# Performance work log

Measured on AMD Instinct MI355X. Metric: run time of the kernel, lower is better.

## Reference

```python
import jax, jax.numpy as jnp
import numpy as np

H = 512      # hidden_size (encoder_embed_dim)
K = 2        # kernel_size (neighbor window)
EPS = 1e-5   # LayerNorm eps

def _ln(x, g, b):
    m = jnp.mean(x, axis=-1, keepdims=True)
    v = jnp.mean(jnp.square(x - m), axis=-1, keepdims=True)
    return (x - m) * jax.lax.rsqrt(v + EPS) * g + b

def _shift_before(h, step):
    # pad `step` zero frames at the front of the seq dim (torch get_hidden_states_before)
    return jnp.pad(h, ((0, 0), (step, 0), (0, 0)))[:, :h.shape[1], :]

def _shift_after(h, step):
    # pad `step` zero frames at the end (torch get_hidden_states_after)
    return jnp.pad(h, ((0, 0), (0, step), (0, 0)))[:, step:, :]

def setup_inputs() -> dict:
    key = jax.random.key(0)
    ks = jax.random.split(key, 12)
    B, S = 32, 256
    s = 0.1  # module init: normal(mean=0, std=0.1)
    return {
        "word_inputs": jax.random.normal(ks[0], (B, S, H), jnp.float32),
        "mask": jnp.zeros((B, S), jnp.int32),  # 1 = padding
        "Wg": jax.random.normal(ks[1], (3 * H, 7 * H), jnp.float32) * s,   # norm_gate.weight.T
        "bg": jax.random.normal(ks[2], (7 * H,), jnp.float32) * s,         # norm_gate.bias
        "We_gate": jax.random.normal(ks[3], (H, 7 * H), jnp.float32) * s,  # emb_gate_linear.weight.T
        "We_trans": jax.random.normal(ks[4], (H, H), jnp.float32) * s,     # emb_trans.weight.T
        "be_trans": jax.random.normal(ks[5], (H,), jnp.float32) * s,
        "W1": jax.random.normal(ks[6], (H, 2 * H), jnp.float32) * (1.0 / np.sqrt(H)),
        "b1": jnp.zeros((2 * H,), jnp.float32),
        "W2": jax.random.normal(ks[7], (2 * H, H), jnp.float32) * (1.0 / np.sqrt(2 * H)),
        "b2": jnp.zeros((H,), jnp.float32),
        # LayerNorm params, order: f1, f2, f3, i, l(e), o, h_LN
        "ln_gamma": jnp.ones((7, H), jnp.float32),
        "ln_beta": jnp.zeros((7, H), jnp.float32),
        "num_layers": 7,
    }

def reference(word_inputs, mask, Wg, bg, We_gate, We_trans, be_trans,
              W1, b1, W2, b2, ln_gamma, ln_beta, num_layers):
    seq_mask = (1.0 - mask.astype(word_inputs.dtype))[..., None]  # [B,S,1]
    x = word_inputs * seq_mask                                    # filtered inputs
    h = x
    c = x
    # computed once outside the recurrent loop, as in the torch module
    we_cat = jnp.einsum('bsh,hg->bsg', x, We_gate)                        # [B,S,7H]
    emb_trans = jnp.tanh(jnp.einsum('bsh,hk->bsk', x, We_trans) + be_trans)
    for _ in range(num_layers):
        hb = sum(_shift_before(h, k + 1) for k in range(K)) * seq_mask    # left-window sum
        ha = sum(_shift_after(h, k + 1) for k in range(K)) * seq_mask     # right-window sum
        cb = sum(_shift_before(c, k + 1) for k in range(K)) * seq_mask
        ca = sum(_shift_after(c, k + 1) for k in range(K)) * seq_mask
        cat = jnp.concatenate([h, hb, ha], axis=-1)                        # [B,S,3H]
        gates = jnp.einsum('bsx,xg->bsg', cat, Wg) + bg + we_cat           # [B,S,7H]
        c_fl, c_fr, c_fc, c_i, c_e, c_w, c_o = jnp.split(gates, 7, axis=-1)
        g_fl = _ln(c_fl, ln_gamma[0], ln_beta[0])
        g_fr = _ln(c_fr, ln_gamma[1], ln_beta[1])
        g_fc = _ln(c_fc, ln_gamma[2], ln_beta[2])
        g_i = jax.nn.sigmoid(_ln(c_i, ln_gamma[3], ln_beta[3]))
        g_e = jax.nn.sigmoid(_ln(c_e, ln_gamma[4], ln_beta[4]))
        g_o = jax.nn.sigmoid(_ln(c_o, ln_gamma[5], ln_beta[5]))
        g_w = jnp.tanh(c_w) + g_e * emb_trans
        f = jax.nn.softmax(jnp.stack([g_fl, g_fr, g_fc], axis=0), axis=0)  # softmax over 3 fgates
        local_c = cb * f[0] + ca * f[1] + c * f[2]
        c = (local_c * (1.0 - g_i) + g_w * g_i) * seq_mask
        h = g_o * jnp.tanh(c) * seq_mask
    hn = _ln(h, ln_gamma[6], ln_beta[6])
    ffn = jnp.einsum('bsk,kh->bsh',
                     jax.nn.relu(jnp.einsum('bsh,hk->bsk', hn, W1) + b1), W2) + b2
    return hn + ffn
```

## Files before the change

### kernel.cpp

```cpp
#include <hip/hip_runtime.h>

#define H 512
#define SEQ 256
#define BATCH 32
#define ROWS (BATCH * SEQ)
#define G7 (7 * H)
#define K3 (3 * H)
#define KC 2048
#define NLAYERS 7
#define LNEPS 1e-5f
#define MCHUNK 4096

typedef __attribute__((ext_vector_type(8))) short s16x8;
typedef __attribute__((ext_vector_type(4))) float f32x4;

__device__ __forceinline__ short f2b(float f) {
  union { float f; unsigned u; } x; x.f = f;
  unsigned r = x.u + 0x7fffu + ((x.u >> 16) & 1u);
  return (short)(r >> 16);
}
__device__ __forceinline__ float b2f(short s) {
  union { unsigned u; float f; } x; x.u = ((unsigned)(unsigned short)s) << 16;
  return x.f;
}

__device__ __forceinline__ void gload_lds16(const void* g, void* l) {
  __builtin_amdgcn_global_load_lds(
      (const __attribute__((address_space(1))) void*)g,
      (__attribute__((address_space(3))) void*)l, 16, 0, 0);
}

#define SFEN() __builtin_amdgcn_sched_barrier(0)
#define SBAR() __builtin_amdgcn_s_barrier()

__global__ __launch_bounds__(256) void make_WgT2(const float* __restrict__ Wg,
                                                 const float* __restrict__ Weg,
                                                 short* __restrict__ out) {
  __shared__ float t[32][33];
  const int nbn = G7 / 32;
  const int bn = blockIdx.x % nbn, bk = blockIdx.x / nbn;
  const int n0 = bn * 32, k0 = bk * 32;
  const int tx = threadIdx.x & 31, ty = threadIdx.x >> 5;
#pragma unroll
  for (int i = 0; i < 4; ++i) {
    const int k = k0 + ty + i * 8;
    t[ty + i * 8][tx] = (k < K3) ? Wg[(long)k * G7 + n0 + tx]
                                 : Weg[(long)(k - K3) * G7 + n0 + tx];
  }
  __syncthreads();
#pragma unroll
  for (int i = 0; i < 4; ++i) {
    const int n = ty + i * 8;
    out[(long)(n0 + n) * KC + k0 + tx] = f2b(t[tx][n]);
  }
}

__global__ __launch_bounds__(256) void trans_w2(const float* __restrict__ in,
                                                short* __restrict__ out,
                                                int Kd, int Nd) {
  __shared__ float t[32][33];
  const int nbn = Nd / 32;
  const int bn = blockIdx.x % nbn, bk = blockIdx.x / nbn;
  const int n0 = bn * 32, k0 = bk * 32;
  const int tx = threadIdx.x & 31, ty = threadIdx.x >> 5;
#pragma unroll
  for (int i = 0; i < 4; ++i)
    t[ty + i * 8][tx] = in[(long)(k0 + ty + i * 8) * Nd + n0 + tx];
  __syncthreads();
#pragma unroll
  for (int i = 0; i < 4; ++i) {
    const int n = ty + i * 8;
    out[(long)(n0 + n) * Kd + k0 + tx] = f2b(t[tx][n]);
  }
}

__global__ void prep(const float* __restrict__ word, const int* __restrict__ mask,
                     float* __restrict__ h, float* __restrict__ c0,
                     short* __restrict__ cat) {
  long i = (long)blockIdx.x * 256 + threadIdx.x;
  int row = (int)(i >> 9);
  int j = (int)(i & (H - 1));
  float msk = mask[row] ? 0.f : 1.f;
  float v = word[i] * msk;
  h[i] = v; c0[i] = v;
  cat[(long)row * KC + K3 + j] = f2b(v);
}

__global__ __launch_bounds__(512) void build_cat(const float* __restrict__ h,
                                                 const int* __restrict__ mask,
                                                 short* __restrict__ cat) {
  int row = blockIdx.x;
  int s = row & (SEQ - 1);
  int j = threadIdx.x;
  float msk = mask[row] ? 0.f : 1.f;
  long rb = (long)row * H + j;
  float v = h[rb];
  float hm1 = (s >= 1) ? h[rb - H] : 0.f;
  float hm2 = (s >= 2) ? h[rb - 2 * H] : 0.f;
  float hp1 = (s <= SEQ - 2) ? h[rb + H] : 0.f;
  float hp2 = (s <= SEQ - 3) ? h[rb + 2 * H] : 0.f;
  long cb = (long)row * KC;
  cat[cb + j] = f2b(v);
  cat[cb + H + j] = f2b((hm1 + hm2) * msk);
  cat[cb + 2 * H + j] = f2b((hp1 + hp2) * msk);
}

#define MFMA16(AF, BF, MOFF)                                              \
  {                                                                       \
    _Pragma("unroll") for (int mf_ = 0; mf_ < 4; ++mf_)                   \
      _Pragma("unroll") for (int nf_ = 0; nf_ < 4; ++nf_)                 \
        acc[(MOFF) + mf_][nf_] = __builtin_amdgcn_mfma_f32_16x16x32_bf16( \
            AF[mf_], BF[nf_], acc[(MOFF) + mf_][nf_], 0, 0, 0);           \
  }

__global__ __launch_bounds__(512) void gemm256_gate(
    const short* __restrict__ A, int lda,
    const short* __restrict__ BT, int ldb,
    int N, int K, const float* __restrict__ bias,
    float* __restrict__ outF) {
  __shared__ __align__(16) short lds[65536];
  const int nbn = N >> 8;
  int bid = blockIdx.x;
  const int nwg = gridDim.x;
  if ((nwg & 7) == 0) {
    const int cpx = nwg >> 3;
    bid = (bid & 7) * cpx + (bid >> 3);
  }
  const int bm = bid / nbn, bn = bid % nbn;
  const int tid = threadIdx.x, lane = tid & 63, wave = tid >> 6;
  const int wm = wave >> 2, wn = wave & 3;
  const int l15 = lane & 15, l4 = lane >> 4;
  const long arow0 = (long)bm * 256, brow0 = (long)bn * 256;
  const int NT = K >> 6;

  f32x4 acc[8][4] = {};

  auto STAGE = [&](int mat, int kh, int tsrc, int sbuf) {
    const short* gb = mat ? BT : A;
    const int ld = mat ? ldb : lda;
    const long r0 = mat ? brow0 : arow0;
    const int kb = tsrc * 64 + kh * 32;
#pragma unroll
    for (int i = 0; i < 2; ++i) {
      const int L16 = i * 512 + tid;
      const int r = L16 >> 2;
      const int cs = ((L16 & 3) << 4) ^ (((r >> 1) & 3) << 4);
      gload_lds16(gb + (r0 + r) * ld + kb + (cs >> 1),
                  lds + sbuf * 32768 + mat * 16384 + kh * 8192 +
                      (i * 512 + (wave << 6)) * 8);
    }
  };
  auto LDA4 = [&](int sbuf, int ks, int mh, s16x8* f) {
#pragma unroll
    for (int mf = 0; mf < 4; ++mf) {
      const int r = wm * 128 + mh * 64 + mf * 16 + l15;
      const int c = (l4 << 4) ^ (((r >> 1) & 3) << 4);
      f[mf] = *(const s16x8*)(lds + sbuf * 32768 + ks * 8192 + r * 32 + (c >> 1));
    }
  };
  auto LDB4 = [&](int sbuf, int ks, s16x8* f) {
#pragma unroll
    for (int nf = 0; nf < 4; ++nf) {
      const int r = wn * 64 + nf * 16 + l15;
      const int c = (l4 << 4) ^ (((r >> 1) & 3) << 4);
      f[nf] = *(const s16x8*)(lds + sbuf * 32768 + 16384 + ks * 8192 + r * 32 + (c >> 1));
    }
  };

  STAGE(0, 0, 0, 0); STAGE(1, 0, 0, 0); STAGE(0, 1, 0, 0); STAGE(1, 1, 0, 0);
  {
    const int t1 = (NT > 1) ? 1 : 0;
    STAGE(0, 0, t1, 1); STAGE(1, 0, t1, 1);
  }
  SFEN();
  asm volatile("s_waitcnt vmcnt(4)" ::: "memory");
  SBAR();
  SFEN();

  for (int t = 0; t < NT; ++t) {
    const int cb = t & 1, nb = cb ^ 1;
    const int t1 = (t + 1 < NT) ? t + 1 : NT - 1;
    const int t2 = (t + 2 < NT) ? t + 2 : NT - 1;
    s16x8 fa[4], fb0[4], fb1[4];

    LDA4(cb, 0, 0, fa); LDB4(cb, 0, fb0);
    STAGE(0, 1, t1, nb);
    SFEN(); SBAR();
    asm volatile("s_waitcnt lgkmcnt(0)" ::: "memory");
    SFEN();
    __builtin_amdgcn_s_setprio(1);
    MFMA16(fa, fb0, 0);
    __builtin_amdgcn_s_setprio(0);
    SFEN(); SBAR(); SFEN();

    LDA4(cb, 0, 1, fa);
    STAGE(1, 1, t1, nb);
    SFEN(); SBAR();
    asm volatile("s_waitcnt lgkmcnt(0)" ::: "memory");
    SFEN();
    __builtin_amdgcn_s_setprio(1);
    MFMA16(fa, fb0, 4);
    __builtin_amdgcn_s_setprio(0);
    SFEN(); SBAR(); SFEN();

    LDA4(cb, 1, 0, fa); LDB4(cb, 1, fb1);
    STAGE(0, 0, t2, cb);
    SFEN(); SBAR();
    asm volatile("s_waitcnt lgkmcnt(0)" ::: "memory");
    SFEN();
    __builtin_amdgcn_s_setprio(1);
    MFMA16(fa, fb1, 0);
    __builtin_amdgcn_s_setprio(0);
    SFEN(); SBAR(); SFEN();

    LDA4(cb, 1, 1, fa);
    STAGE(1, 0, t2, cb);
    SFEN(); SBAR();
    asm volatile("s_waitcnt lgkmcnt(0)" ::: "memory");
    SFEN();
    __builtin_amdgcn_s_setprio(1);
    MFMA16(fa, fb1, 4);
    __builtin_amdgcn_s_setprio(0);
    SFEN();
    asm volatile("s_waitcnt vmcnt(4)" ::: "memory");
    SBAR();
    SFEN();
  }
  asm volatile("s_waitcnt vmcnt(0)" ::: "memory");

#pragma unroll
  for (int mi = 0; mi < 8; ++mi) {
#pragma unroll
    for (int nf = 0; nf < 4; ++nf) {
#pragma unroll
      for (int j = 0; j < 4; ++j) {
        const long row = arow0 + wm * 128 + mi * 16 + l4 * 4 + j;
        const long col = brow0 + wn * 64 + nf * 16 + l15;
        outF[row * N + col] = acc[mi][nf][j] + bias[col];
      }
    }
  }
}

template <int EPI>
__global__ __launch_bounds__(256) void gemm_bt(
    const short* __restrict__ A, int lda, const short* __restrict__ BT,
    int M, int N, int K,
    const float* __restrict__ bias,
    const float* __restrict__ addF,
    float* __restrict__ outF, short* __restrict__ outB) {
  __shared__ __align__(16) short As[128 * 32];
  __shared__ __align__(16) short Bs[128 * 32];
  const int nbn = N >> 7;
  const int bm = blockIdx.x / nbn;
  const int bn = blockIdx.x % nbn;
  const int tid = threadIdx.x;
  const int lane = tid & 63;
  const int wave = tid >> 6;
  const int wr = (wave >> 1) << 6;
  const int wc = (wave & 1) << 6;
  const int l15 = lane & 15;
  const int krow = (lane >> 4) << 3;

  f32x4 acc[4][4] = {};

  const long arow0 = (long)bm * 128;
  const long brow0 = (long)bn * 128;

  for (int k0 = 0; k0 < K; k0 += 32) {
#pragma unroll
    for (int i = 0; i < 2; ++i) {
      const int e = (i * 256 + tid) * 8;
      const int r = e >> 5, c = e & 31;
      gload_lds16(A + (arow0 + r) * lda + k0 + c, As + (long)(i * 256 + (wave << 6)) * 8);
      gload_lds16(BT + (brow0 + r) * K + k0 + c, Bs + (long)(i * 256 + (wave << 6)) * 8);
    }
    __syncthreads();
    s16x8 af[4], bfr[4];
#pragma unroll
    for (int m = 0; m < 4; ++m)
      af[m] = *(const s16x8*)(As + (wr + m * 16 + l15) * 32 + krow);
#pragma unroll
    for (int n = 0; n < 4; ++n)
      bfr[n] = *(const s16x8*)(Bs + (wc + n * 16 + l15) * 32 + krow);
#pragma unroll
    for (int m = 0; m < 4; ++m)
#pragma unroll
      for (int n = 0; n < 4; ++n)
        acc[m][n] = __builtin_amdgcn_mfma_f32_16x16x32_bf16(af[m], bfr[n], acc[m][n], 0, 0, 0);
    __syncthreads();
  }

#pragma unroll
  for (int m = 0; m < 4; ++m) {
#pragma unroll
    for (int n = 0; n < 4; ++n) {
#pragma unroll
      for (int j = 0; j < 4; ++j) {
        const long row = arow0 + wr + m * 16 + ((lane >> 4) << 2) + j;
        const long col = brow0 + wc + n * 16 + l15;
        const float v = acc[m][n][j];
        if (EPI == 0) {
          outB[row * N + col] = f2b(tanhf(v + bias[col]));
        } else if (EPI == 2) {
          outB[row * N + col] = f2b(fmaxf(v + bias[col], 0.f));
        } else {
          outF[row * N + col] = v + bias[col] + addF[row * N + col];
        }
      }
    }
  }
}

__global__ __launch_bounds__(512) void pointwise(
    const float* __restrict__ gates, const short* __restrict__ emb,
    const float* __restrict__ cin, float* __restrict__ cout,
    float* __restrict__ h, const int* __restrict__ mask,
    const float* __restrict__ lng, const float* __restrict__ lnb, int row0) {
  const int row = row0 + blockIdx.x;
  const int s = row & (SEQ - 1);
  const int tid = threadIdx.x;
  const int lane = tid & 63, wave = tid >> 6;
  const float msk = mask[row] ? 0.f : 1.f;
  const float* grow = gates + (long)blockIdx.x * G7;

  float g[7];
#pragma unroll
  for (int k = 0; k < 7; ++k) g[k] = grow[k * H + tid];

  const int cidx[6] = {0, 1, 2, 3, 4, 6};
  float red[12];
#pragma unroll
  for (int i = 0; i < 6; ++i) {
    float v = g[cidx[i]];
    red[i] = v; red[6 + i] = v * v;
  }
#pragma unroll
  for (int st = 32; st > 0; st >>= 1) {
#pragma unroll
    for (int i = 0; i < 12; ++i) red[i] += __shfl_xor(red[i], st, 64);
  }
  __shared__ float lred[8][12];
  __shared__ float fin[12];
  if (lane == 0) {
#pragma unroll
    for (int i = 0; i < 12; ++i) lred[wave][i] = red[i];
  }
  __syncthreads();
  if (tid < 12) {
    float a = 0.f;
#pragma unroll
    for (int w = 0; w < 8; ++w) a += lred[w][tid];
    fin[tid] = a;
  }
  __syncthreads();

  float ln[6];
#pragma unroll
  for (int i = 0; i < 6; ++i) {
    float mean = fin[i] * (1.f / (float)H);
    float var = fin[6 + i] * (1.f / (float)H) - mean * mean;
    float inv = rsqrtf(var + LNEPS);
    int pidx = (i < 5) ? i : 5;
    ln[i] = (g[cidx[i]] - mean) * inv * lng[pidx * H + tid] + lnb[pidx * H + tid];
  }
  float gfl = ln[0], gfr = ln[1], gfc = ln[2];
  float gi = 1.f / (1.f + expf(-ln[3]));
  float ge = 1.f / (1.f + expf(-ln[4]));
  float go = 1.f / (1.f + expf(-ln[5]));
  float gw = tanhf(g[5]) + ge * b2f(emb[(long)row * H + tid]);

  float mx = fmaxf(gfl, fmaxf(gfr, gfc));
  float e0 = expf(gfl - mx), e1 = expf(gfr - mx), e2 = expf(gfc - mx);
  float inv3 = 1.f / (e0 + e1 + e2);
  float f0 = e0 * inv3, f1 = e1 * inv3, f2 = e2 * inv3;

  const long rb = (long)row * H + tid;
  float cc = cin[rb];
  float cm1 = (s >= 1) ? cin[rb - H] : 0.f;
  float cm2 = (s >= 2) ? cin[rb - 2 * H] : 0.f;
  float cp1 = (s <= SEQ - 2) ? cin[rb + H] : 0.f;
  float cp2 = (s <= SEQ - 3) ? cin[rb + 2 * H] : 0.f;
  float cbv = (cm1 + cm2) * msk, cav = (cp1 + cp2) * msk;
  float lc = cbv * f0 + cav * f1 + cc * f2;
  float cn = (lc * (1.f - gi) + gw * gi) * msk;
  float hv = go * tanhf(cn) * msk;
  cout[rb] = cn;
  h[rb] = hv;
}

__global__ __launch_bounds__(512) void ln_final(
    const float* __restrict__ h, const float* __restrict__ g6,
    const float* __restrict__ b6, float* __restrict__ hnF,
    short* __restrict__ hnB) {
  const int row = blockIdx.x;
  const int tid = threadIdx.x;
  const int lane = tid & 63, wave = tid >> 6;
  const long rb = (long)row * H + tid;
  float v = h[rb];
  float r0 = v, r1 = v * v;
#pragma unroll
  for (int st = 32; st > 0; st >>= 1) {
    r0 += __shfl_xor(r0, st, 64);
    r1 += __shfl_xor(r1, st, 64);
  }
  __shared__ float lred[8][2];
  __shared__ float fin[2];
  if (lane == 0) { lred[wave][0] = r0; lred[wave][1] = r1; }
  __syncthreads();
  if (tid < 2) {
    float a = 0.f;
#pragma unroll
    for (int w = 0; w < 8; ++w) a += lred[w][tid];
    fin[tid] = a;
  }
  __syncthreads();
  float mean = fin[0] * (1.f / (float)H);
  float var = fin[1] * (1.f / (float)H) - mean * mean;
  float inv = rsqrtf(var + LNEPS);
  float o = (v - mean) * inv * g6[tid] + b6[tid];
  hnF[rb] = o;
  hnB[rb] = f2b(o);
}

extern "C" void kernel_launch(void* const* d_in, const int* in_sizes, int n_in,
                              void* d_out, int out_size, void* d_ws, size_t ws_size,
                              hipStream_t stream) {
  const float* word = (const float*)d_in[0];
  const int* mask = (const int*)d_in[1];
  const float* Wg = (const float*)d_in[2];
  const float* bg = (const float*)d_in[3];
  const float* We_gate = (const float*)d_in[4];
  const float* We_trans = (const float*)d_in[5];
  const float* be_trans = (const float*)d_in[6];
  const float* W1 = (const float*)d_in[7];
  const float* b1 = (const float*)d_in[8];
  const float* W2 = (const float*)d_in[9];
  const float* b2 = (const float*)d_in[10];
  const float* ln_g = (const float*)d_in[11];
  const float* ln_b = (const float*)d_in[12];
  float* out = (float*)d_out;

  char* p = (char*)d_ws;
  auto take = [&](size_t bytes) -> char* {
    char* r = p;
    p += (bytes + 255) & ~(size_t)255;
    return r;
  };
  short* WgT   = (short*)take((size_t)G7 * KC * 2);
  short* WeTt  = (short*)take((size_t)H * H * 2);
  short* W1T   = (short*)take((size_t)(2 * H) * H * 2);
  short* W2T   = (short*)take((size_t)H * (2 * H) * 2);
  short* cat   = (short*)take((size_t)ROWS * KC * 2);
  float* gates = (float*)take((size_t)MCHUNK * G7 * 4);
  short* emb   = (short*)take((size_t)ROWS * H * 2);
  float* h     = (float*)take((size_t)ROWS * H * 4);
  float* c0    = (float*)take((size_t)ROWS * H * 4);
  float* c1    = (float*)take((size_t)ROWS * H * 4);
  float* hnF = c0;
  short* hnB = emb;
  short* t1  = (short*)gates;

  {
    long n = (long)G7 * KC;
    make_WgT2<<<(int)(n / (32 * 32)), 256, 0, stream>>>(Wg, We_gate, WgT);
    n = (long)H * H;
    trans_w2<<<(int)(n / (32 * 32)), 256, 0, stream>>>(We_trans, WeTt, H, H);
    n = (long)H * 2 * H;
    trans_w2<<<(int)(n / (32 * 32)), 256, 0, stream>>>(W1, W1T, H, 2 * H);
    n = (long)2 * H * H;
    trans_w2<<<(int)(n / (32 * 32)), 256, 0, stream>>>(W2, W2T, 2 * H, H);
  }

  prep<<<ROWS * H / 256, 256, 0, stream>>>(word, mask, h, c0, cat);

  gemm_bt<0><<<(ROWS / 128) * (H / 128), 256, 0, stream>>>(
      cat + K3, KC, WeTt, ROWS, H, H, be_trans, nullptr, nullptr, emb);

  float* cin = c0;
  float* cout = c1;
  for (int l = 0; l < NLAYERS; ++l) {
    build_cat<<<ROWS, 512, 0, stream>>>(h, mask, cat);
    for (int ch = 0; ch < ROWS / MCHUNK; ++ch) {
      gemm256_gate<<<(MCHUNK / 256) * (G7 / 256), 512, 0, stream>>>(
          cat + (long)ch * MCHUNK * KC, KC, WgT, KC, G7, KC, bg, gates);
      pointwise<<<MCHUNK, 512, 0, stream>>>(gates, emb, cin, cout, h, mask,
                                            ln_g, ln_b, ch * MCHUNK);
    }
    float* tmp = cin; cin = cout; cout = tmp;
  }

  ln_final<<<ROWS, 512, 0, stream>>>(h, ln_g + 6 * H, ln_b + 6 * H, hnF, hnB);
  gemm_bt<2><<<(ROWS / 128) * ((2 * H) / 128), 256, 0, stream>>>(
      hnB, H, W1T, ROWS, 2 * H, H, b1, nullptr, nullptr, t1);
  gemm_bt<3><<<(ROWS / 128) * (H / 128), 256, 0, stream>>>(
      t1, 2 * H, W2T, ROWS, H, 2 * H, b2, hnF, out, nullptr);
}
```

Measured before the change: 1.708 ms.

## Merge weight transposes, restructure gate GEMM pipeline, and use full-size gate chunk

Combines the four weight-transpose launches into one kernel that selects its source by block index. Reworks the gate GEMM main loop so two stage loads are issued together and the second A fragment load sits between MFMA groups, halving the number of barriers per k-step. Makes the gate chunk size depend on workspace size, so when the workspace is large enough all 8192 rows run in one GEMM and pointwise launch per layer. The trade-offs are higher register pressure from the extra fragment buffer and possible LDS hazards from fewer barriers.

```diff
diff --git a/kernel.cpp b/kernel.cpp
--- a/kernel.cpp
+++ b/kernel.cpp
@@ -9,7 +9,6 @@
 #define KC 2048
 #define NLAYERS 7
 #define LNEPS 1e-5f
-#define MCHUNK 4096
 
 typedef __attribute__((ext_vector_type(8))) short s16x8;
 typedef __attribute__((ext_vector_type(4))) float f32x4;
@@ -33,44 +32,34 @@
 #define SFEN() __builtin_amdgcn_sched_barrier(0)
 #define SBAR() __builtin_amdgcn_s_barrier()
 
-__global__ __launch_bounds__(256) void make_WgT2(const float* __restrict__ Wg,
-                                                 const float* __restrict__ Weg,
-                                                 short* __restrict__ out) {
+__global__ __launch_bounds__(256) void trans_fused(
+    const float* __restrict__ Wg, const float* __restrict__ Weg,
+    const float* __restrict__ Wet, const float* __restrict__ W1,
+    const float* __restrict__ W2,
+    short* __restrict__ WgT, short* __restrict__ WeTt,
+    short* __restrict__ W1T, short* __restrict__ W2T) {
   __shared__ float t[32][33];
-  const int nbn = G7 / 32;
-  const int bn = blockIdx.x % nbn, bk = blockIdx.x / nbn;
+  int b = blockIdx.x;
+  const float *s1, *s2; short* o; int Kd, Nd, bound;
+  if (b < 7168)      { s1 = Wg;  s2 = Weg; o = WgT;  Kd = KC;   Nd = G7;   bound = K3; }
+  else if (b < 7424) { b -= 7168; s1 = s2 = Wet; o = WeTt; Kd = 512;  Nd = 512;  bound = 1 << 30; }
+  else if (b < 7936) { b -= 7424; s1 = s2 = W1;  o = W1T;  Kd = 512;  Nd = 1024; bound = 1 << 30; }
+  else               { b -= 7936; s1 = s2 = W2;  o = W2T;  Kd = 1024; Nd = 512;  bound = 1 << 30; }
+  const int nbn = Nd / 32;
+  const int bn = b % nbn, bk = b / nbn;
   const int n0 = bn * 32, k0 = bk * 32;
   const int tx = threadIdx.x & 31, ty = threadIdx.x >> 5;
 #pragma unroll
   for (int i = 0; i < 4; ++i) {
     const int k = k0 + ty + i * 8;
-    t[ty + i * 8][tx] = (k < K3) ? Wg[(long)k * G7 + n0 + tx]
-                                 : Weg[(long)(k - K3) * G7 + n0 + tx];
+    t[ty + i * 8][tx] = (k < bound) ? s1[(long)k * Nd + n0 + tx]
+                                    : s2[(long)(k - K3) * Nd + n0 + tx];
   }
   __syncthreads();
 #pragma unroll
   for (int i = 0; i < 4; ++i) {
     const int n = ty + i * 8;
-    out[(long)(n0 + n) * KC + k0 + tx] = f2b(t[tx][n]);
-  }
-}
-
-__global__ __launch_bounds__(256) void trans_w2(const float* __restrict__ in,
-                                                short* __restrict__ out,
-                                                int Kd, int Nd) {
-  __shared__ float t[32][33];
-  const int nbn = Nd / 32;
-  const int bn = blockIdx.x % nbn, bk = blockIdx.x / nbn;
-  const int n0 = bn * 32, k0 = bk * 32;
-  const int tx = threadIdx.x & 31, ty = threadIdx.x >> 5;
-#pragma unroll
-  for (int i = 0; i < 4; ++i)
-    t[ty + i * 8][tx] = in[(long)(k0 + ty + i * 8) * Nd + n0 + tx];
-  __syncthreads();
-#pragma unroll
-  for (int i = 0; i < 4; ++i) {
-    const int n = ty + i * 8;
-    out[(long)(n0 + n) * Kd + k0 + tx] = f2b(t[tx][n]);
+    o[(long)(n0 + n) * Kd + k0 + tx] = f2b(t[tx][n]);
   }
 }
 
@@ -169,8 +158,8 @@
 
   STAGE(0, 0, 0, 0); STAGE(1, 0, 0, 0); STAGE(0, 1, 0, 0); STAGE(1, 1, 0, 0);
   {
-    const int t1 = (NT > 1) ? 1 : 0;
-    STAGE(0, 0, t1, 1); STAGE(1, 0, t1, 1);
+    const int t1p = (NT > 1) ? 1 : 0;
+    STAGE(0, 0, t1p, 1); STAGE(1, 0, t1p, 1);
   }
   SFEN();
   asm volatile("s_waitcnt vmcnt(4)" ::: "memory");
@@ -181,45 +170,29 @@
     const int cb = t & 1, nb = cb ^ 1;
     const int t1 = (t + 1 < NT) ? t + 1 : NT - 1;
     const int t2 = (t + 2 < NT) ? t + 2 : NT - 1;
-    s16x8 fa[4], fb0[4], fb1[4];
-
-    LDA4(cb, 0, 0, fa); LDB4(cb, 0, fb0);
-    STAGE(0, 1, t1, nb);
-    SFEN(); SBAR();
+    s16x8 fa[4], fa2[4], fb[4];
+
+    LDA4(cb, 0, 0, fa); LDB4(cb, 0, fb);
+    STAGE(0, 1, t1, nb); STAGE(1, 1, t1, nb);
+    SFEN();
     asm volatile("s_waitcnt lgkmcnt(0)" ::: "memory");
     SFEN();
     __builtin_amdgcn_s_setprio(1);
-    MFMA16(fa, fb0, 0);
+    MFMA16(fa, fb, 0);
+    LDA4(cb, 0, 1, fa2);
+    MFMA16(fa2, fb, 4);
     __builtin_amdgcn_s_setprio(0);
     SFEN(); SBAR(); SFEN();
 
-    LDA4(cb, 0, 1, fa);
-    STAGE(1, 1, t1, nb);
-    SFEN(); SBAR();
+    LDA4(cb, 1, 0, fa); LDB4(cb, 1, fb);
+    STAGE(0, 0, t2, cb); STAGE(1, 0, t2, cb);
+    SFEN();
     asm volatile("s_waitcnt lgkmcnt(0)" ::: "memory");
     SFEN();
     __builtin_amdgcn_s_setprio(1);
-    MFMA16(fa, fb0, 4);
-    __builtin_amdgcn_s_setprio(0);
-    SFEN(); SBAR(); SFEN();
-
-    LDA4(cb, 1, 0, fa); LDB4(cb, 1, fb1);
-    STAGE(0, 0, t2, cb);
-    SFEN(); SBAR();
-    asm volatile("s_waitcnt lgkmcnt(0)" ::: "memory");
-    SFEN();
-    __builtin_amdgcn_s_setprio(1);
-    MFMA16(fa, fb1, 0);
-    __builtin_amdgcn_s_setprio(0);
-    SFEN(); SBAR(); SFEN();
-
-    LDA4(cb, 1, 1, fa);
-    STAGE(1, 0, t2, cb);
-    SFEN(); SBAR();
-    asm volatile("s_waitcnt lgkmcnt(0)" ::: "memory");
-    SFEN();
-    __builtin_amdgcn_s_setprio(1);
-    MFMA16(fa, fb1, 4);
+    MFMA16(fa, fb, 0);
+    LDA4(cb, 1, 1, fa2);
+    MFMA16(fa2, fb, 4);
     __builtin_amdgcn_s_setprio(0);
     SFEN();
     asm volatile("s_waitcnt vmcnt(4)" ::: "memory");
@@ -441,6 +414,8 @@
   const float* ln_b = (const float*)d_in[12];
   float* out = (float*)d_out;
 
+  const int mchunk = (ws_size >= (size_t)228 * 1024 * 1024) ? ROWS : ROWS / 2;
+
   char* p = (char*)d_ws;
   auto take = [&](size_t bytes) -> char* {
     char* r = p;
@@ -452,7 +427,7 @@
   short* W1T   = (short*)take((size_t)(2 * H) * H * 2);
   short* W2T   = (short*)take((size_t)H * (2 * H) * 2);
   short* cat   = (short*)take((size_t)ROWS * KC * 2);
-  float* gates = (float*)take((size_t)MCHUNK * G7 * 4);
+  float* gates = (float*)take((size_t)mchunk * G7 * 4);
   short* emb   = (short*)take((size_t)ROWS * H * 2);
   float* h     = (float*)take((size_t)ROWS * H * 4);
   float* c0    = (float*)take((size_t)ROWS * H * 4);
@@ -461,16 +436,8 @@
   short* hnB = emb;
   short* t1  = (short*)gates;
 
-  {
-    long n = (long)G7 * KC;
-    make_WgT2<<<(int)(n / (32 * 32)), 256, 0, stream>>>(Wg, We_gate, WgT);
-    n = (long)H * H;
-    trans_w2<<<(int)(n / (32 * 32)), 256, 0, stream>>>(We_trans, WeTt, H, H);
-    n = (long)H * 2 * H;
-    trans_w2<<<(int)(n / (32 * 32)), 256, 0, stream>>>(W1, W1T, H, 2 * H);
-    n = (long)2 * H * H;
-    trans_w2<<<(int)(n / (32 * 32)), 256, 0, stream>>>(W2, W2T, 2 * H, H);
-  }
+  trans_fused<<<8448, 256, 0, stream>>>(Wg, We_gate, We_trans, W1, W2,
+                                        WgT, WeTt, W1T, W2T);
 
   prep<<<ROWS * H / 256, 256, 0, stream>>>(word, mask, h, c0, cat);
 
@@ -481,11 +448,11 @@
   float* cout = c1;
   for (int l = 0; l < NLAYERS; ++l) {
     build_cat<<<ROWS, 512, 0, stream>>>(h, mask, cat);
-    for (int ch = 0; ch < ROWS / MCHUNK; ++ch) {
-      gemm256_gate<<<(MCHUNK / 256) * (G7 / 256), 512, 0, stream>>>(
-          cat + (long)ch * MCHUNK * KC, KC, WgT, KC, G7, KC, bg, gates);
-      pointwise<<<MCHUNK, 512, 0, stream>>>(gates, emb, cin, cout, h, mask,
-                                            ln_g, ln_b, ch * MCHUNK);
+    for (int ch = 0; ch < ROWS / mchunk; ++ch) {
+      gemm256_gate<<<(mchunk / 256) * (G7 / 256), 512, 0, stream>>>(
+          cat + (long)ch * mchunk * KC, KC, WgT, KC, G7, KC, bg, gates);
+      pointwise<<<mchunk, 512, 0, stream>>>(gates, emb, cin, cout, h, mask,
+                                            ln_g, ln_b, ch * mchunk);
     }
     float* tmp = cin; cin = cout; cout = tmp;
   }
```

Result: faster. 1.610 ms (-5.7%).
